# Optimization experiments

Hardware: AMD Instinct MI355X
Metric: run time of the kernel (lower is better)

## Reference

```python
import jax, jax.numpy as jnp
import numpy as np


def setup_inputs() -> dict:
    key = jax.random.key(0)
    k1, k2, k3 = jax.random.split(key, 3)
    B, S, N = 32, 128, 256
    input_real = jax.random.normal(k1, (B, S, N), dtype=jnp.float32)
    input_imag = jax.random.normal(k2, (B, S, N), dtype=jnp.float32)
    weight = jax.random.uniform(k3, (B, S), dtype=jnp.float32)
    return {"input_real": input_real, "input_imag": input_imag, "weight": weight}


def reference(input_real, input_imag, weight):
    # Weighted mixture of rank-1 density matrices over the sequence dim S.
    # output_real[b,n,m] = sum_s w[b,s] * (r[b,s,n]*r[b,s,m] + i[b,s,n]*i[b,s,m])
    # output_imag[b,n,m] = sum_s w[b,s] * (i[b,s,n]*r[b,s,m] - r[b,s,n]*i[b,s,m])
    # Fused: pre-scale one factor by the weight, then a single contraction over S
    # (never materializes the [B,S,N,N] intermediates of the torch code).
    wr = input_real * weight[:, :, None]  # [B,S,N]
    wi = input_imag * weight[:, :, None]  # [B,S,N]
    output_r = jnp.einsum('bsn,bsm->bnm', wr, input_real) + jnp.einsum('bsn,bsm->bnm', wi, input_imag)
    output_i = jnp.einsum('bsn,bsm->bnm', wi, input_real) - jnp.einsum('bsn,bsm->bnm', wr, input_imag)
    return (output_r, output_i)
```

## Files before the change

### kernel.cpp

```cpp
#include <hip/hip_runtime.h>
#include <hip/hip_fp16.h>


constexpr int B = 32, S = 128, N = 256;

typedef _Float16 f16x8 __attribute__((ext_vector_type(8)));
typedef float    f32x4 __attribute__((ext_vector_type(4)));

union F16x8 { f16x8 v; __half2 h2[4]; };

__global__ __launch_bounds__(512, 4) void ComplexMixture_71313636983193_kernel(
    const float* __restrict__ R, const float* __restrict__ I,
    const float* __restrict__ W, float* __restrict__ Or, float* __restrict__ Oi)
{
    __shared__ alignas(16) _Float16 T[4][64][128];

    const int pb   = blockIdx.x;
    const int lbid = (pb & 7) * 64 + (pb >> 3);
    const int b  = lbid >> 4;
    const int ti = (lbid >> 2) & 3;
    const int tj = lbid & 3;
    const int t  = threadIdx.x;
    const int wv = t >> 6, lane = t & 63;

    const float* Wb = W + b * S;
    const size_t bb = (size_t)b * S * N;
    const float* baseR[2] = { R + bb + ti * 64, R + bb + tj * 64 };
    const float* baseI[2] = { I + bb + ti * 64, I + bb + tj * 64 };

    #pragma unroll
    for (int pass = 0; pass < 2; ++pass) {
        const int task  = t + pass * 512;
        const int npair = task & 31;
        const int octet = (task >> 5) & 15;
        const int side  = task >> 9;
        const int s0    = octet * 8;

        const float* pR = baseR[side] + npair * 2;
        const float* pI = baseI[side] + npair * 2;

        float2 r2[8], i2[8];
        #pragma unroll
        for (int s = 0; s < 8; ++s) {
            r2[s] = *(const float2*)&pR[(size_t)(s0 + s) * N];
            i2[s] = *(const float2*)&pI[(size_t)(s0 + s) * N];
        }

        float w8[8];
        if (side == 0) {
            #pragma unroll
            for (int s = 0; s < 8; ++s) w8[s] = Wb[s0 + s];
        }

        const int slot = octet ^ (npair & 7);
        #pragma unroll
        for (int j = 0; j < 2; ++j) {
            const int n = npair * 2 + j;
            F16x8 fr, fi;
            if (side == 0) {
                #pragma unroll
                for (int k = 0; k < 4; ++k) {
                    const float a0 = j ? r2[2*k].y : r2[2*k].x;
                    const float a1 = j ? r2[2*k+1].y : r2[2*k+1].x;
                    const float c0 = j ? i2[2*k].y : i2[2*k].x;
                    const float c1 = j ? i2[2*k+1].y : i2[2*k+1].x;
                    fr.h2[k] = __floats2half2_rn(w8[2*k] * a0, w8[2*k+1] * a1);
                    fi.h2[k] = __floats2half2_rn(w8[2*k] * c0, w8[2*k+1] * c1);
                }
            } else {
                #pragma unroll
                for (int k = 0; k < 4; ++k) {
                    const float a0 = j ? r2[2*k].y : r2[2*k].x;
                    const float a1 = j ? r2[2*k+1].y : r2[2*k+1].x;
                    const float c0 = j ? i2[2*k].y : i2[2*k].x;
                    const float c1 = j ? i2[2*k+1].y : i2[2*k+1].x;
                    fr.h2[k] = __floats2half2_rn(a0, a1);
                    fi.h2[k] = __floats2half2_rn(c0, c1);
                }
            }
            *(f16x8*)&T[side * 2 + 0][n][slot * 8] = fr.v;
            *(f16x8*)&T[side * 2 + 1][n][slot * 8] = fi.v;
        }
    }
    __syncthreads();

    const int wn = (wv & 3) * 16;
    const int wm = (wv >> 2) * 32;
    const int fr16 = lane & 15, kb = lane >> 4;
    const int ra = wn + fr16;

    f32x4 accR[2] = {}, accA[2] = {}, accB[2] = {};

    __builtin_amdgcn_s_setprio(1);
    #pragma unroll
    for (int ks = 0; ks < 4; ++ks) {
        const int K  = ks * 4 + kb;
        const int ca = (K ^ ((ra >> 1) & 7)) * 8;
        const f16x8 awr = *(const f16x8*)&T[0][ra][ca];
        const f16x8 awi = *(const f16x8*)&T[1][ra][ca];
        #pragma unroll
        for (int ms = 0; ms < 2; ++ms) {
            const int rb = wm + ms * 16 + fr16;
            const int cb = (K ^ ((rb >> 1) & 7)) * 8;
            const f16x8 br = *(const f16x8*)&T[2][rb][cb];
            const f16x8 bi = *(const f16x8*)&T[3][rb][cb];
            accR[ms] = __builtin_amdgcn_mfma_f32_16x16x32_f16(awr, br, accR[ms], 0, 0, 0);
            accR[ms] = __builtin_amdgcn_mfma_f32_16x16x32_f16(awi, bi, accR[ms], 0, 0, 0);
            accA[ms] = __builtin_amdgcn_mfma_f32_16x16x32_f16(awi, br, accA[ms], 0, 0, 0);
            accB[ms] = __builtin_amdgcn_mfma_f32_16x16x32_f16(awr, bi, accB[ms], 0, 0, 0);
        }
    }
    __builtin_amdgcn_s_setprio(0);

    const int n0 = ti * 64, m0 = tj * 64;
    const int nn = n0 + wn + kb * 4;
    #pragma unroll
    for (int ms = 0; ms < 2; ++ms) {
        const int mm = m0 + wm + ms * 16 + fr16;
        #pragma unroll
        for (int r = 0; r < 4; ++r) {
            const size_t o = ((size_t)b * N + nn + r) * N + mm;
            Or[o] = accR[ms][r];
            Oi[o] = accA[ms][r] - accB[ms][r];
        }
    }
}

extern "C" void kernel_launch(void* const* d_in, const int* in_sizes, int n_in,
                              void* d_out, int out_size, void* d_ws, size_t ws_size,
                              hipStream_t stream) {
    const float* R = (const float*)d_in[0];
    const float* I = (const float*)d_in[1];
    const float* W = (const float*)d_in[2];
    float* Or = (float*)d_out;
    float* Oi = (float*)d_out + (size_t)B * N * N;

    ComplexMixture_71313636983193_kernel<<<dim3(512), dim3(512), 0, stream>>>(
        R, I, W, Or, Oi);
}
```

Before: 13.89 us.

## Split S-dimension staging into two halves and overlap with MFMA compute and stores

```diff
diff --git a/kernel.cpp b/kernel.cpp
--- a/kernel.cpp
+++ b/kernel.cpp
@@ -8,6 +8,8 @@
 typedef float    f32x4 __attribute__((ext_vector_type(4)));
 
 union F16x8 { f16x8 v; __half2 h2[4]; };
+
+#define MFMA16(a, bv, c) __builtin_amdgcn_mfma_f32_16x16x32_f16((a), (bv), (c), 0, 0, 0)
 
 __global__ __launch_bounds__(512, 4) void ComplexMixture_71313636983193_kernel(
     const float* __restrict__ R, const float* __restrict__ I,
@@ -23,107 +25,123 @@
     const int t  = threadIdx.x;
     const int wv = t >> 6, lane = t & 63;
 
-    const float* Wb = W + b * S;
+    const int nquad = t & 15;
+    const int octet = (t >> 4) & 7;
+    const int side  = (t >> 7) & 1;
+    const int arr   = t >> 8;
+
     const size_t bb = (size_t)b * S * N;
-    const float* baseR[2] = { R + bb + ti * 64, R + bb + tj * 64 };
-    const float* baseI[2] = { I + bb + ti * 64, I + bb + tj * 64 };
+    const int chunk = side ? tj : ti;
+    const float* src = (arr ? I : R) + bb + chunk * 64 + nquad * 4;
+    const float* Wb  = W + b * S;
+
+    _Float16 (* const Td)[128] = T[side * 2 + arr];
+
+    float4 f0[8];
+    #pragma unroll
+    for (int s = 0; s < 8; ++s)
+        f0[s] = *(const float4*)&src[(size_t)(octet * 8 + s) * N];
+
+    float w0[8], w1[8];
+    if (side == 0) {
+        const float4 a0 = *(const float4*)&Wb[octet * 8];
+        const float4 a1 = *(const float4*)&Wb[octet * 8 + 4];
+        const float4 a2 = *(const float4*)&Wb[64 + octet * 8];
+        const float4 a3 = *(const float4*)&Wb[64 + octet * 8 + 4];
+        w0[0]=a0.x; w0[1]=a0.y; w0[2]=a0.z; w0[3]=a0.w;
+        w0[4]=a1.x; w0[5]=a1.y; w0[6]=a1.z; w0[7]=a1.w;
+        w1[0]=a2.x; w1[1]=a2.y; w1[2]=a2.z; w1[3]=a2.w;
+        w1[4]=a3.x; w1[5]=a3.y; w1[6]=a3.z; w1[7]=a3.w;
+    }
 
     #pragma unroll
-    for (int pass = 0; pass < 2; ++pass) {
-        const int task  = t + pass * 512;
-        const int npair = task & 31;
-        const int octet = (task >> 5) & 15;
-        const int side  = task >> 9;
-        const int s0    = octet * 8;
+    for (int j = 0; j < 4; ++j) {
+        const int n    = nquad * 4 + j;
+        const int slot = octet ^ ((n >> 1) & 7);
+        F16x8 f;
+        #pragma unroll
+        for (int k = 0; k < 4; ++k) {
+            float lo = ((const float*)&f0[2 * k])[j];
+            float hi = ((const float*)&f0[2 * k + 1])[j];
+            if (side == 0) { lo *= w0[2 * k]; hi *= w0[2 * k + 1]; }
+            f.h2[k] = __floats2half2_rn(lo, hi);
+        }
+        *(f16x8*)&Td[n][slot * 8] = f.v;
+    }
 
-        const float* pR = baseR[side] + npair * 2;
-        const float* pI = baseI[side] + npair * 2;
+    float4 f1[8];
+    #pragma unroll
+    for (int s = 0; s < 8; ++s)
+        f1[s] = *(const float4*)&src[(size_t)(64 + octet * 8 + s) * N];
 
-        float2 r2[8], i2[8];
-        #pragma unroll
-        for (int s = 0; s < 8; ++s) {
-            r2[s] = *(const float2*)&pR[(size_t)(s0 + s) * N];
-            i2[s] = *(const float2*)&pI[(size_t)(s0 + s) * N];
-        }
-
-        float w8[8];
-        if (side == 0) {
-            #pragma unroll
-            for (int s = 0; s < 8; ++s) w8[s] = Wb[s0 + s];
-        }
-
-        const int slot = octet ^ (npair & 7);
-        #pragma unroll
-        for (int j = 0; j < 2; ++j) {
-            const int n = npair * 2 + j;
-            F16x8 fr, fi;
-            if (side == 0) {
-                #pragma unroll
-                for (int k = 0; k < 4; ++k) {
-                    const float a0 = j ? r2[2*k].y : r2[2*k].x;
-                    const float a1 = j ? r2[2*k+1].y : r2[2*k+1].x;
-                    const float c0 = j ? i2[2*k].y : i2[2*k].x;
-                    const float c1 = j ? i2[2*k+1].y : i2[2*k+1].x;
-                    fr.h2[k] = __floats2half2_rn(w8[2*k] * a0, w8[2*k+1] * a1);
-                    fi.h2[k] = __floats2half2_rn(w8[2*k] * c0, w8[2*k+1] * c1);
-                }
-            } else {
-                #pragma unroll
-                for (int k = 0; k < 4; ++k) {
-                    const float a0 = j ? r2[2*k].y : r2[2*k].x;
-                    const float a1 = j ? r2[2*k+1].y : r2[2*k+1].x;
-                    const float c0 = j ? i2[2*k].y : i2[2*k].x;
-                    const float c1 = j ? i2[2*k+1].y : i2[2*k+1].x;
-                    fr.h2[k] = __floats2half2_rn(a0, a1);
-                    fi.h2[k] = __floats2half2_rn(c0, c1);
-                }
-            }
-            *(f16x8*)&T[side * 2 + 0][n][slot * 8] = fr.v;
-            *(f16x8*)&T[side * 2 + 1][n][slot * 8] = fi.v;
-        }
-    }
     __syncthreads();
 
     const int wn = (wv & 3) * 16;
     const int wm = (wv >> 2) * 32;
     const int fr16 = lane & 15, kb = lane >> 4;
-    const int ra = wn + fr16;
+    const int ra  = wn + fr16;          const int sa  = (ra  >> 1) & 7;
+    const int rb0 = wm + fr16;          const int sb0 = (rb0 >> 1) & 7;
+    const int rb1 = wm + 16 + fr16;     const int sb1 = (rb1 >> 1) & 7;
 
     f32x4 accR[2] = {}, accA[2] = {}, accB[2] = {};
+    f16x8 awr, awi;
+
+#define LOAD_A(ks) { const int ca = (((ks) * 4 + kb) ^ sa) * 8;              \
+        awr = *(const f16x8*)&T[0][ra][ca];                                  \
+        awi = *(const f16x8*)&T[1][ra][ca]; }
+#define STEP_B(ks, ms) { const int K = (ks) * 4 + kb;                        \
+        const int rb = (ms) ? rb1 : rb0;                                     \
+        const int cb = (K ^ ((ms) ? sb1 : sb0)) * 8;                         \
+        const f16x8 br = *(const f16x8*)&T[2][rb][cb];                       \
+        const f16x8 bi = *(const f16x8*)&T[3][rb][cb];                       \
+        accR[ms] = MFMA16(awr, br, accR[ms]);                                \
+        accR[ms] = MFMA16(awi, bi, accR[ms]);                                \
+        accA[ms] = MFMA16(awi, br, accA[ms]);                                \
+        accB[ms] = MFMA16(awr, bi, accB[ms]); }
 
     __builtin_amdgcn_s_setprio(1);
+    LOAD_A(0); STEP_B(0, 0); STEP_B(0, 1);
+    LOAD_A(1); STEP_B(1, 0); STEP_B(1, 1);
+    __builtin_amdgcn_s_setprio(0);
+
     #pragma unroll
-    for (int ks = 0; ks < 4; ++ks) {
-        const int K  = ks * 4 + kb;
-        const int ca = (K ^ ((ra >> 1) & 7)) * 8;
-        const f16x8 awr = *(const f16x8*)&T[0][ra][ca];
-        const f16x8 awi = *(const f16x8*)&T[1][ra][ca];
+    for (int j = 0; j < 4; ++j) {
+        const int n    = nquad * 4 + j;
+        const int slot = (8 + octet) ^ ((n >> 1) & 7);
+        F16x8 f;
         #pragma unroll
-        for (int ms = 0; ms < 2; ++ms) {
-            const int rb = wm + ms * 16 + fr16;
-            const int cb = (K ^ ((rb >> 1) & 7)) * 8;
-            const f16x8 br = *(const f16x8*)&T[2][rb][cb];
-            const f16x8 bi = *(const f16x8*)&T[3][rb][cb];
-            accR[ms] = __builtin_amdgcn_mfma_f32_16x16x32_f16(awr, br, accR[ms], 0, 0, 0);
-            accR[ms] = __builtin_amdgcn_mfma_f32_16x16x32_f16(awi, bi, accR[ms], 0, 0, 0);
-            accA[ms] = __builtin_amdgcn_mfma_f32_16x16x32_f16(awi, br, accA[ms], 0, 0, 0);
-            accB[ms] = __builtin_amdgcn_mfma_f32_16x16x32_f16(awr, bi, accB[ms], 0, 0, 0);
+        for (int k = 0; k < 4; ++k) {
+            float lo = ((const float*)&f1[2 * k])[j];
+            float hi = ((const float*)&f1[2 * k + 1])[j];
+            if (side == 0) { lo *= w1[2 * k]; hi *= w1[2 * k + 1]; }
+            f.h2[k] = __floats2half2_rn(lo, hi);
         }
+        *(f16x8*)&Td[n][slot * 8] = f.v;
     }
-    __builtin_amdgcn_s_setprio(0);
+
+    __syncthreads();
 
     const int n0 = ti * 64, m0 = tj * 64;
     const int nn = n0 + wn + kb * 4;
-    #pragma unroll
-    for (int ms = 0; ms < 2; ++ms) {
-        const int mm = m0 + wm + ms * 16 + fr16;
-        #pragma unroll
-        for (int r = 0; r < 4; ++r) {
-            const size_t o = ((size_t)b * N + nn + r) * N + mm;
-            Or[o] = accR[ms][r];
-            Oi[o] = accA[ms][r] - accB[ms][r];
-        }
-    }
+
+#define STORE_MS(ms) {                                                       \
+        const int mm = m0 + wm + (ms) * 16 + fr16;                           \
+        _Pragma("unroll")                                                    \
+        for (int r = 0; r < 4; ++r) {                                        \
+            const size_t o = ((size_t)b * N + nn + r) * N + mm;              \
+            Or[o] = accR[ms][r];                                             \
+            Oi[o] = accA[ms][r] - accB[ms][r];                               \
+        } }
+
+    __builtin_amdgcn_s_setprio(1);
+    LOAD_A(2); STEP_B(2, 0); STEP_B(2, 1);
+    LOAD_A(3); STEP_B(3, 0);
+    __builtin_amdgcn_s_setprio(0);
+    STORE_MS(0);
+    __builtin_amdgcn_s_setprio(1);
+    STEP_B(3, 1);
+    __builtin_amdgcn_s_setprio(0);
+    STORE_MS(1);
 }
 
 extern "C" void kernel_launch(void* const* d_in, const int* in_sizes, int n_in,
```

Measured after the change: 12.99 us. -6.4%, faster.
